# Performance work log

Hardware: AMD Instinct MI355X
Metric: run time of the kernel (lower is better)

The kernel has to match this reference:

```python
import jax, jax.numpy as jnp
import numpy as np

C = 256  # channels
B, H, W = 16, 64, 64


def _conv1x1(x, w, b):
    # x: [B,Cin,H,W], w: [Cout,Cin], b: [Cout] -> [B,Cout,H,W]
    return jnp.einsum('bchw,oc->bohw', x, w) + b[None, :, None, None]


def _axis_attn(x, wq, bq, wf, bf, axis):
    # axis: -1 for 'W', -2 for 'H'
    qkv = _conv1x1(x, wq, bq)                      # [B,1+2C,H,W]
    query = qkv[:, :1]                             # [B,1,H,W]
    key = qkv[:, 1:1 + C]                          # [B,C,H,W]
    value = qkv[:, 1 + C:]                         # [B,C,H,W]
    scores = jax.nn.softmax(query, axis=axis)      # softmax over spatial axis
    context = jnp.sum(key * scores, axis=axis, keepdims=True)  # [B,C,H,1] or [B,C,1,W]
    gate = jax.nn.sigmoid(value)
    out = x + gate * context                       # broadcast over reduced axis
    return _conv1x1(out, wf, bf)


def setup_inputs() -> dict:
    key = jax.random.key(0)
    ks = jax.random.split(key, 5)
    s_qkv = 1.0 / np.sqrt(C)
    s_fus = 1.0 / np.sqrt(C)
    return {
        'x': jax.random.normal(ks[0], (B, C, H, W), dtype=jnp.float32),
        'qkvW_w': jax.random.normal(ks[1], (1 + 2 * C, C), dtype=jnp.float32) * s_qkv,
        'qkvW_b': jnp.zeros((1 + 2 * C,), dtype=jnp.float32),
        'qkvH_w': jax.random.normal(ks[2], (1 + 2 * C, C), dtype=jnp.float32) * s_qkv,
        'qkvH_b': jnp.zeros((1 + 2 * C,), dtype=jnp.float32),
        'fusW_w': jax.random.normal(ks[3], (C, C), dtype=jnp.float32) * s_fus,
        'fusW_b': jnp.zeros((C,), dtype=jnp.float32),
        'fusH_w': jax.random.normal(ks[4], (C, C), dtype=jnp.float32) * s_fus,
        'fusH_b': jnp.zeros((C,), dtype=jnp.float32),
    }


def reference(x, qkvW_w, qkvW_b, qkvH_w, qkvH_b, fusW_w, fusW_b, fusH_w, fusH_b):
    x_w = _axis_attn(x, qkvW_w, qkvW_b, fusW_w, fusW_b, axis=-1)
    x_h = _axis_attn(x_w, qkvH_w, qkvH_b, fusH_w, fusH_b, axis=-2)
    return x_h
```

## Files before the change

### kernel.cpp

```cpp
#include <hip/hip_runtime.h>

typedef unsigned short u16;
typedef unsigned int u32;
typedef __attribute__((ext_vector_type(8))) short bf16x8;
typedef __attribute__((ext_vector_type(4))) float f32x4;

__device__ __forceinline__ u16 f2bf(float f) {
    u32 u = __builtin_bit_cast(u32, f);
    u += 0x7FFFu + ((u >> 16) & 1u);
    return (u16)(u >> 16);
}
__device__ __forceinline__ float bf2f(u16 s) {
    u32 u = ((u32)s) << 16;
    return __builtin_bit_cast(float, u);
}
__device__ __forceinline__ float sigm(float x) {
    return 1.0f / (1.0f + __expf(-x));
}
__device__ __forceinline__ void gload16(const u16* g, u16* l) {
    __builtin_amdgcn_global_load_lds(
        (const __attribute__((address_space(1))) void*)g,
        (__attribute__((address_space(3))) void*)l, 16, 0, 0);
}

__global__ __launch_bounds__(256) void transpose_in(const float* __restrict__ x,
                                                    u16* __restrict__ xp) {
    __shared__ float tile[64][65];
    int bid = blockIdx.x;
    int ct = bid & 3, h = (bid >> 2) & 63, b = bid >> 8;
    int t = threadIdx.x;
    int tr = t >> 4, tc = t & 15;
    const float* src = x + (((size_t)(b * 256 + ct * 64) * 64 + h) * 64);
#pragma unroll
    for (int i = 0; i < 4; ++i) {
        int c = tr + i * 16;
        float4 v = *(const float4*)(src + (size_t)c * 4096 + tc * 4);
        tile[c][tc * 4 + 0] = v.x;
        tile[c][tc * 4 + 1] = v.y;
        tile[c][tc * 4 + 2] = v.z;
        tile[c][tc * 4 + 3] = v.w;
    }
    __syncthreads();
    u16* dst = xp + ((size_t)((b * 64 + h) * 64)) * 256 + ct * 64;
#pragma unroll
    for (int i = 0; i < 4; ++i) {
        int w = tr + i * 16;
        ushort4 o;
        o.x = f2bf(tile[tc * 4 + 0][w]);
        o.y = f2bf(tile[tc * 4 + 1][w]);
        o.z = f2bf(tile[tc * 4 + 2][w]);
        o.w = f2bf(tile[tc * 4 + 3][w]);
        *(ushort4*)(dst + (size_t)w * 256 + tc * 4) = o;
    }
}

__global__ __launch_bounds__(256) void prep_w(const float* __restrict__ qw,
                                              const float* __restrict__ qb,
                                              const float* __restrict__ fw,
                                              const float* __restrict__ fb,
                                              float* __restrict__ wq0,
                                              u16* __restrict__ wkv,
                                              float* __restrict__ bkv,
                                              u16* __restrict__ wf,
                                              float* __restrict__ bff) {
    int i = blockIdx.x * 256 + threadIdx.x;
    if (i < 513 * 256) {
        int o = i >> 8, c = i & 255;
        float v = qw[i];
        if (o == 0) wq0[c] = v;
        else        wkv[(size_t)(o - 1) * 256 + c] = f2bf(v);
    }
    if (i < 65536) wf[i] = f2bf(fw[i]);
    if (i < 512)   bkv[i] = qb[i + 1];
    if (i < 256)   bff[i] = fb[i];
}

template <int AXIS>
__global__ __launch_bounds__(512, 2) void qkv_attn(
    const u16* __restrict__ A, const u16* __restrict__ Bw,
    const float* __restrict__ bkv, const float* __restrict__ wq0,
    u16* __restrict__ G) {
    __shared__ alignas(16) u16 Asm[128 * 256];
    __shared__ alignas(16) u16 Bsm[128 * 256];
    __shared__ float ql[128];
    __shared__ float sc[128];
    __shared__ float ctxs[2][256];
    int t = threadIdx.x, lane = t & 63, wv = t >> 6;
    int beta = blockIdx.x;
    auto prow = [&](int r) -> size_t {
        if (AXIS == 0) return (size_t)beta * 128 + r;
        else           return (size_t)(beta >> 5) * 4096 + (size_t)(r & 63) * 64 +
                              ((beta & 31) * 2) + (r >> 6);
    };
    {
        int r5 = t >> 5, c5 = t & 31;
#pragma unroll
        for (int i = 0; i < 8; ++i) {
            int row = i * 16 + r5;
            int slot = c5 ^ (row & 7);
            gload16(A + prow(row) * 256 + slot * 8, &Asm[(i * 16 + wv * 2) * 256]);
        }
    }
    __syncthreads();
    {
        int row = t >> 2, g = t & 3;
        const float* wp = wq0 + g * 64;
        float a = 0.f;
#pragma unroll
        for (int cc = 0; cc < 8; ++cc) {
            int slot = (g * 8 + cc) ^ (row & 7);
            bf16x8 v = *(const bf16x8*)&Asm[row * 256 + slot * 8];
#pragma unroll
            for (int j = 0; j < 8; ++j) a += bf2f((u16)v[j]) * wp[cc * 8 + j];
        }
        a += __shfl_xor(a, 1);
        a += __shfl_xor(a, 2);
        if (g == 0) ql[row] = a;
    }
    __syncthreads();
    if (t < 128) {
        float qv = ql[t];
        float m = qv;
#pragma unroll
        for (int off = 32; off > 0; off >>= 1) m = fmaxf(m, __shfl_xor(m, off));
        float e = __expf(qv - m);
        float s = e;
#pragma unroll
        for (int off = 32; off > 0; off >>= 1) s += __shfl_xor(s, off);
        sc[t] = e / s;
    }
    int wm = (wv & 1) * 64, wn = (wv >> 1) * 32;
    int arow = lane & 15, kgrp = lane >> 4, l7 = lane & 7;
    int line = wv & 1;
    for (int ot = 0; ot < 4; ++ot) {
        __syncthreads();
        {
            int r5 = t >> 5, c5 = t & 31;
#pragma unroll
            for (int i = 0; i < 8; ++i) {
                int row = i * 16 + r5;
                int slot = c5 ^ (row & 7);
                gload16(Bw + (size_t)(ot * 128 + row) * 256 + slot * 8,
                        &Bsm[(i * 16 + wv * 2) * 256]);
            }
        }
        __syncthreads();
        f32x4 zero = {0.f, 0.f, 0.f, 0.f};
        f32x4 acc[4][2];
#pragma unroll
        for (int mi = 0; mi < 4; ++mi) {
            acc[mi][0] = zero;
            acc[mi][1] = zero;
        }
#pragma unroll
        for (int ks = 0; ks < 8; ++ks) {
            int soff = ((ks * 4 + kgrp) ^ l7) * 8;
            bf16x8 af[4], bf[2];
#pragma unroll
            for (int mi = 0; mi < 4; ++mi)
                af[mi] = *(const bf16x8*)&Asm[(wm + mi * 16 + arow) * 256 + soff];
#pragma unroll
            for (int ni = 0; ni < 2; ++ni)
                bf[ni] = *(const bf16x8*)&Bsm[(wn + ni * 16 + arow) * 256 + soff];
#pragma unroll
            for (int mi = 0; mi < 4; ++mi)
#pragma unroll
                for (int ni = 0; ni < 2; ++ni)
                    acc[mi][ni] = __builtin_amdgcn_mfma_f32_16x16x32_bf16(
                        af[mi], bf[ni], acc[mi][ni], 0, 0, 0);
        }
        if (ot < 2) {
#pragma unroll
            for (int ni = 0; ni < 2; ++ni) {
                int col = ot * 128 + wn + ni * 16 + arow;
                float part = 0.f;
#pragma unroll
                for (int mi = 0; mi < 4; ++mi) {
                    int rbase = wm + mi * 16 + kgrp * 4;
#pragma unroll
                    for (int r = 0; r < 4; ++r)
                        part += acc[mi][ni][r] * sc[rbase + r];
                }
                part += __shfl_xor(part, 16);
                part += __shfl_xor(part, 32);
                if (lane < 16) ctxs[line][col] = part + bkv[col];
            }
        } else {
#pragma unroll
            for (int ni = 0; ni < 2; ++ni) {
                int c = (ot - 2) * 128 + wn + ni * 16 + arow;
                float bv = bkv[256 + c];
                float cx = ctxs[line][c];
#pragma unroll
                for (int mi = 0; mi < 4; ++mi) {
#pragma unroll
                    for (int r = 0; r < 4; ++r) {
                        int row = wm + mi * 16 + kgrp * 4 + r;
                        float v = acc[mi][ni][r] + bv;
                        int slot = (c >> 3) ^ (row & 7);
                        float xv = bf2f(Asm[row * 256 + slot * 8 + (c & 7)]);
                        G[prow(row) * 256 + c] = f2bf(xv + sigm(v) * cx);
                    }
                }
            }
        }
    }
}

template <int MODE>
__global__ __launch_bounds__(256, 2) void gemm_k(
    const u16* __restrict__ A, const u16* __restrict__ Bw,
    const float* __restrict__ bias,
    u16* __restrict__ bOut, float* __restrict__ fOut) {
    int h = blockIdx.x;
    int xcd = h & 7, slot = h >> 3;
    int otile = slot & 1, ptile = xcd * 64 + (slot >> 1);
    __shared__ alignas(16) u16 Asm[128 * 64];
    __shared__ alignas(16) u16 Bsm[128 * 64];
    int p0 = ptile * 128, o0 = otile * 128;
    int t = threadIdx.x, lane = t & 63, wv = t >> 6;
    int wm = (wv >> 1) * 64, wn = (wv & 1) * 64;
    int l7 = lane & 7;
    int srcoff = (lane >> 3) * 256 + (((lane & 7) ^ (lane >> 3)) * 8);
    int arow = lane & 15, kgrp = lane >> 4;
    f32x4 zero = {0.f, 0.f, 0.f, 0.f};
    f32x4 acc[4][4];
#pragma unroll
    for (int i = 0; i < 4; ++i)
#pragma unroll
        for (int jj = 0; jj < 4; ++jj) acc[i][jj] = zero;

    for (int k0 = 0; k0 < 256; k0 += 64) {
        __syncthreads();
#pragma unroll
        for (int it = 0; it < 4; ++it) {
            int r0 = it * 32 + wv * 8;
            gload16(A + (size_t)(p0 + r0) * 256 + k0 + srcoff, &Asm[r0 * 64]);
            gload16(Bw + (size_t)(o0 + r0) * 256 + k0 + srcoff, &Bsm[r0 * 64]);
        }
        __syncthreads();
#pragma unroll
        for (int kk = 0; kk < 64; kk += 32) {
            int soff = (((kk >> 3) + kgrp) ^ l7) << 3;
            bf16x8 af[4], bfv[4];
#pragma unroll
            for (int mi = 0; mi < 4; ++mi)
                af[mi] = *(const bf16x8*)&Asm[(wm + mi * 16 + arow) * 64 + soff];
#pragma unroll
            for (int ni = 0; ni < 4; ++ni)
                bfv[ni] = *(const bf16x8*)&Bsm[(wn + ni * 16 + arow) * 64 + soff];
#pragma unroll
            for (int mi = 0; mi < 4; ++mi)
#pragma unroll
                for (int ni = 0; ni < 4; ++ni)
                    acc[mi][ni] = __builtin_amdgcn_mfma_f32_16x16x32_bf16(
                        af[mi], bfv[ni], acc[mi][ni], 0, 0, 0);
        }
    }
#pragma unroll
    for (int mi = 0; mi < 4; ++mi) {
#pragma unroll
        for (int ni = 0; ni < 4; ++ni) {
            int col = o0 + wn + ni * 16 + arow;
            float bv = bias[col];
#pragma unroll
            for (int r = 0; r < 4; ++r) {
                int row = p0 + wm + mi * 16 + ((lane >> 4) << 2) + r;
                float v = acc[mi][ni][r] + bv;
                if (MODE == 1) {
                    bOut[(size_t)row * 256 + col] = f2bf(v);
                } else {
                    fOut[((size_t)((row >> 12) * 256 + col)) * 4096 + (row & 4095)] = v;
                }
            }
        }
    }
}

extern "C" void kernel_launch(void* const* d_in, const int* in_sizes, int n_in,
                              void* d_out, int out_size, void* d_ws, size_t ws_size,
                              hipStream_t stream) {
    const float* x   = (const float*)d_in[0];
    const float* qWw = (const float*)d_in[1];
    const float* qWb = (const float*)d_in[2];
    const float* qHw = (const float*)d_in[3];
    const float* qHb = (const float*)d_in[4];
    const float* fWw = (const float*)d_in[5];
    const float* fWb = (const float*)d_in[6];
    const float* fHw = (const float*)d_in[7];
    const float* fHb = (const float*)d_in[8];
    float* out = (float*)d_out;

    char* ws = (char*)d_ws;
    size_t off = 0;
    auto carve = [&](size_t bytes) -> void* {
        off = (off + 255) & ~(size_t)255;
        void* p = ws + off;
        off += bytes;
        return p;
    };
    const size_t P = 65536;
    u16*   xp  = (u16*)carve(P * 256 * 2);
    u16*   kb  = (u16*)carve(P * 256 * 2);
    u16*   vb  = (u16*)carve(P * 256 * 2);
    float* wq01 = (float*)carve(256 * 4);
    u16*   wkv1 = (u16*)carve(512 * 256 * 2);
    float* bkv1 = (float*)carve(512 * 4);
    u16*   wf1  = (u16*)carve(65536 * 2);
    float* bf1  = (float*)carve(256 * 4);
    float* wq02 = (float*)carve(256 * 4);
    u16*   wkv2 = (u16*)carve(512 * 256 * 2);
    float* bkv2 = (float*)carve(512 * 4);
    u16*   wf2  = (u16*)carve(65536 * 2);
    float* bf2  = (float*)carve(256 * 4);

    prep_w<<<513, 256, 0, stream>>>(qWw, qWb, fWw, fWb, wq01, wkv1, bkv1, wf1, bf1);
    prep_w<<<513, 256, 0, stream>>>(qHw, qHb, fHw, fHb, wq02, wkv2, bkv2, wf2, bf2);
    transpose_in<<<4096, 256, 0, stream>>>(x, xp);

    qkv_attn<0><<<512, 512, 0, stream>>>(xp, wkv1, bkv1, wq01, kb);
    gemm_k<1><<<1024, 256, 0, stream>>>(kb, wf1, bf1, vb, nullptr);
    qkv_attn<1><<<512, 512, 0, stream>>>(vb, wkv2, bkv2, wq02, kb);
    gemm_k<2><<<1024, 256, 0, stream>>>(kb, wf2, bf2, nullptr, out);
    (void)in_sizes; (void)n_in; (void)out_size; (void)ws_size;
}
```

Baseline: 160.6 us.

## Stream qkv weights from global memory and transpose MFMA operand roles in qkv_attn

Removes the 64KB shared-memory weight tile and the per-output-tile weight staging and barriers. Each wave now reads its weight fragments straight from global (L2-cached) memory as the MFMA A operand, with pixels as the B operand. This gives 4 consecutive channels per lane, so the gate epilogue can use vectorized ushort4 stores and f32x4 bias/context loads. Shared memory roughly halves, so launch bounds now ask for 4 blocks per CU. The trade-off is uncoalesced, latency-bound global loads inside the MFMA loop instead of LDS reads, and more registers spent on the transposed accumulator layout.

```diff
diff --git a/kernel.cpp b/kernel.cpp
--- a/kernel.cpp
+++ b/kernel.cpp
@@ -76,15 +76,14 @@
 }
 
 template <int AXIS>
-__global__ __launch_bounds__(512, 2) void qkv_attn(
+__global__ __launch_bounds__(512, 4) void qkv_attn(
     const u16* __restrict__ A, const u16* __restrict__ Bw,
     const float* __restrict__ bkv, const float* __restrict__ wq0,
     u16* __restrict__ G) {
     __shared__ alignas(16) u16 Asm[128 * 256];
-    __shared__ alignas(16) u16 Bsm[128 * 256];
     __shared__ float ql[128];
     __shared__ float sc[128];
-    __shared__ float ctxs[2][256];
+    __shared__ alignas(16) float ctxs[2][256];
     int t = threadIdx.x, lane = t & 63, wv = t >> 6;
     int beta = blockIdx.x;
     auto prow = [&](int r) -> size_t {
@@ -93,11 +92,10 @@
                               ((beta & 31) * 2) + (r >> 6);
     };
     {
-        int r5 = t >> 5, c5 = t & 31;
 #pragma unroll
         for (int i = 0; i < 8; ++i) {
-            int row = i * 16 + r5;
-            int slot = c5 ^ (row & 7);
+            int row = i * 16 + wv * 2 + (lane >> 5);
+            int slot = (lane & 31) ^ (row & 7);
             gload16(A + prow(row) * 256 + slot * 8, &Asm[(i * 16 + wv * 2) * 256]);
         }
     }
@@ -129,81 +127,84 @@
         for (int off = 32; off > 0; off >>= 1) s += __shfl_xor(s, off);
         sc[t] = e / s;
     }
-    int wm = (wv & 1) * 64, wn = (wv >> 1) * 32;
-    int arow = lane & 15, kgrp = lane >> 4, l7 = lane & 7;
-    int line = wv & 1;
+    __syncthreads();
+    int rowhalf = wv >> 2, chq = wv & 3;
+    int arow = lane & 15, kgrp = lane >> 4;
+    float sv[4];
+#pragma unroll
+    for (int ni = 0; ni < 4; ++ni) sv[ni] = sc[rowhalf * 64 + ni * 16 + arow];
     for (int ot = 0; ot < 4; ++ot) {
-        __syncthreads();
-        {
-            int r5 = t >> 5, c5 = t & 31;
-#pragma unroll
-            for (int i = 0; i < 8; ++i) {
-                int row = i * 16 + r5;
-                int slot = c5 ^ (row & 7);
-                gload16(Bw + (size_t)(ot * 128 + row) * 256 + slot * 8,
-                        &Bsm[(i * 16 + wv * 2) * 256]);
+        f32x4 zero = {0.f, 0.f, 0.f, 0.f};
+        f32x4 acc[2][4];
+#pragma unroll
+        for (int mi = 0; mi < 2; ++mi)
+#pragma unroll
+            for (int ni = 0; ni < 4; ++ni) acc[mi][ni] = zero;
+#pragma unroll
+        for (int ks = 0; ks < 8; ++ks) {
+            bf16x8 aw[2], bx[4];
+#pragma unroll
+            for (int mi = 0; mi < 2; ++mi)
+                aw[mi] = *(const bf16x8*)(Bw +
+                    (size_t)(ot * 128 + chq * 32 + mi * 16 + arow) * 256 +
+                    ks * 32 + kgrp * 8);
+#pragma unroll
+            for (int ni = 0; ni < 4; ++ni) {
+                int p = rowhalf * 64 + ni * 16 + arow;
+                int slot = (ks * 4 + kgrp) ^ (p & 7);
+                bx[ni] = *(const bf16x8*)&Asm[p * 256 + slot * 8];
             }
-        }
-        __syncthreads();
-        f32x4 zero = {0.f, 0.f, 0.f, 0.f};
-        f32x4 acc[4][2];
-#pragma unroll
-        for (int mi = 0; mi < 4; ++mi) {
-            acc[mi][0] = zero;
-            acc[mi][1] = zero;
-        }
-#pragma unroll
-        for (int ks = 0; ks < 8; ++ks) {
-            int soff = ((ks * 4 + kgrp) ^ l7) * 8;
-            bf16x8 af[4], bf[2];
-#pragma unroll
-            for (int mi = 0; mi < 4; ++mi)
-                af[mi] = *(const bf16x8*)&Asm[(wm + mi * 16 + arow) * 256 + soff];
-#pragma unroll
-            for (int ni = 0; ni < 2; ++ni)
-                bf[ni] = *(const bf16x8*)&Bsm[(wn + ni * 16 + arow) * 256 + soff];
-#pragma unroll
-            for (int mi = 0; mi < 4; ++mi)
-#pragma unroll
-                for (int ni = 0; ni < 2; ++ni)
+#pragma unroll
+            for (int mi = 0; mi < 2; ++mi)
+#pragma unroll
+                for (int ni = 0; ni < 4; ++ni)
                     acc[mi][ni] = __builtin_amdgcn_mfma_f32_16x16x32_bf16(
-                        af[mi], bf[ni], acc[mi][ni], 0, 0, 0);
+                        aw[mi], bx[ni], acc[mi][ni], 0, 0, 0);
         }
         if (ot < 2) {
 #pragma unroll
-            for (int ni = 0; ni < 2; ++ni) {
-                int col = ot * 128 + wn + ni * 16 + arow;
-                float part = 0.f;
-#pragma unroll
-                for (int mi = 0; mi < 4; ++mi) {
-                    int rbase = wm + mi * 16 + kgrp * 4;
-#pragma unroll
-                    for (int r = 0; r < 4; ++r)
-                        part += acc[mi][ni][r] * sc[rbase + r];
+            for (int mi = 0; mi < 2; ++mi) {
+                int c = ot * 128 + chq * 32 + mi * 16 + kgrp * 4;
+                f32x4 red;
+#pragma unroll
+                for (int r = 0; r < 4; ++r) {
+                    float s = 0.f;
+#pragma unroll
+                    for (int ni = 0; ni < 4; ++ni) s += acc[mi][ni][r] * sv[ni];
+                    s += __shfl_xor(s, 1);
+                    s += __shfl_xor(s, 2);
+                    s += __shfl_xor(s, 4);
+                    s += __shfl_xor(s, 8);
+                    red[r] = s;
                 }
-                part += __shfl_xor(part, 16);
-                part += __shfl_xor(part, 32);
-                if (lane < 16) ctxs[line][col] = part + bkv[col];
+                if (arow == 0) {
+                    f32x4 bv = *(const f32x4*)&bkv[c];
+                    red[0] += bv[0]; red[1] += bv[1];
+                    red[2] += bv[2]; red[3] += bv[3];
+                    *(f32x4*)&ctxs[rowhalf][c] = red;
+                }
             }
         } else {
 #pragma unroll
-            for (int ni = 0; ni < 2; ++ni) {
-                int c = (ot - 2) * 128 + wn + ni * 16 + arow;
-                float bv = bkv[256 + c];
-                float cx = ctxs[line][c];
-#pragma unroll
-                for (int mi = 0; mi < 4; ++mi) {
-#pragma unroll
-                    for (int r = 0; r < 4; ++r) {
-                        int row = wm + mi * 16 + kgrp * 4 + r;
-                        float v = acc[mi][ni][r] + bv;
-                        int slot = (c >> 3) ^ (row & 7);
-                        float xv = bf2f(Asm[row * 256 + slot * 8 + (c & 7)]);
-                        G[prow(row) * 256 + c] = f2bf(xv + sigm(v) * cx);
-                    }
+            for (int mi = 0; mi < 2; ++mi) {
+                int cv = (ot - 2) * 128 + chq * 32 + mi * 16 + kgrp * 4;
+                f32x4 bv = *(const f32x4*)&bkv[256 + cv];
+                f32x4 cxv = *(const f32x4*)&ctxs[rowhalf][cv];
+#pragma unroll
+                for (int ni = 0; ni < 4; ++ni) {
+                    int p = rowhalf * 64 + ni * 16 + arow;
+                    int slot = (cv >> 3) ^ (p & 7);
+                    ushort4 xv = *(const ushort4*)&Asm[p * 256 + slot * 8 + (cv & 7)];
+                    ushort4 o;
+                    o.x = f2bf(bf2f(xv.x) + sigm(acc[mi][ni][0] + bv[0]) * cxv[0]);
+                    o.y = f2bf(bf2f(xv.y) + sigm(acc[mi][ni][1] + bv[1]) * cxv[1]);
+                    o.z = f2bf(bf2f(xv.z) + sigm(acc[mi][ni][2] + bv[2]) * cxv[2]);
+                    o.w = f2bf(bf2f(xv.w) + sigm(acc[mi][ni][3] + bv[3]) * cxv[3]);
+                    *(ushort4*)(G + prow(p) * 256 + cv) = o;
                 }
             }
         }
+        if (ot == 1) __syncthreads();
     }
 }
 
```

New measurement: 159.1 us. No clear change (-0.9%).

## Compute attention context algebraically via softmax-weighted x then key weights

Applied to the files above, without the earlier changes.

Replaces the fused qkv_attn kernel with two kernels. line_ctx uses linearity: it first forms the softmax-weighted sum of x per line, then applies the key weights as a matrix-vector product, so the full key GEMM is never computed. val_gate then runs only the value GEMM with an MFMA-tiled loop and applies the sigmoid gate using the context read back from global memory. The change removes half the GEMM FLOPs in the attention stage, at the cost of an extra kernel launch, a second read of the activations and a small context buffer.

```diff
diff --git a/kernel.cpp b/kernel.cpp
--- a/kernel.cpp
+++ b/kernel.cpp
@@ -76,30 +76,25 @@
 }
 
 template <int AXIS>
-__global__ __launch_bounds__(512, 2) void qkv_attn(
-    const u16* __restrict__ A, const u16* __restrict__ Bw,
-    const float* __restrict__ bkv, const float* __restrict__ wq0,
-    u16* __restrict__ G) {
-    __shared__ alignas(16) u16 Asm[128 * 256];
-    __shared__ alignas(16) u16 Bsm[128 * 256];
-    __shared__ float ql[128];
-    __shared__ float sc[128];
-    __shared__ float ctxs[2][256];
+__global__ __launch_bounds__(256) void line_ctx(
+    const u16* __restrict__ A, const u16* __restrict__ Wk,
+    const float* __restrict__ wq0, const float* __restrict__ bkv,
+    float* __restrict__ ctx) {
+    __shared__ alignas(16) u16 Xl[64 * 256];
+    __shared__ float ql[64];
+    __shared__ float sc[64];
+    __shared__ alignas(16) float ys[256];
     int t = threadIdx.x, lane = t & 63, wv = t >> 6;
-    int beta = blockIdx.x;
+    int l = blockIdx.x;
     auto prow = [&](int r) -> size_t {
-        if (AXIS == 0) return (size_t)beta * 128 + r;
-        else           return (size_t)(beta >> 5) * 4096 + (size_t)(r & 63) * 64 +
-                              ((beta & 31) * 2) + (r >> 6);
+        if (AXIS == 0) return (size_t)l * 64 + r;
+        else           return (size_t)(l >> 6) * 4096 + (size_t)r * 64 + (l & 63);
     };
-    {
-        int r5 = t >> 5, c5 = t & 31;
-#pragma unroll
-        for (int i = 0; i < 8; ++i) {
-            int row = i * 16 + r5;
-            int slot = c5 ^ (row & 7);
-            gload16(A + prow(row) * 256 + slot * 8, &Asm[(i * 16 + wv * 2) * 256]);
-        }
+#pragma unroll
+    for (int i = 0; i < 8; ++i) {
+        int row = i * 8 + wv * 2 + (lane >> 5);
+        int slot = (lane & 31) ^ (row & 7);
+        gload16(A + prow(row) * 256 + slot * 8, &Xl[(i * 8 + wv * 2) * 256]);
     }
     __syncthreads();
     {
@@ -109,7 +104,7 @@
 #pragma unroll
         for (int cc = 0; cc < 8; ++cc) {
             int slot = (g * 8 + cc) ^ (row & 7);
-            bf16x8 v = *(const bf16x8*)&Asm[row * 256 + slot * 8];
+            bf16x8 v = *(const bf16x8*)&Xl[row * 256 + slot * 8];
 #pragma unroll
             for (int j = 0; j < 8; ++j) a += bf2f((u16)v[j]) * wp[cc * 8 + j];
         }
@@ -118,7 +113,7 @@
         if (g == 0) ql[row] = a;
     }
     __syncthreads();
-    if (t < 128) {
+    if (t < 64) {
         float qv = ql[t];
         float m = qv;
 #pragma unroll
@@ -129,79 +124,95 @@
         for (int off = 32; off > 0; off >>= 1) s += __shfl_xor(s, off);
         sc[t] = e / s;
     }
-    int wm = (wv & 1) * 64, wn = (wv >> 1) * 32;
-    int arow = lane & 15, kgrp = lane >> 4, l7 = lane & 7;
-    int line = wv & 1;
-    for (int ot = 0; ot < 4; ++ot) {
+    __syncthreads();
+    {
+        int chunk = t >> 3, e7 = t & 7;
+        float a = 0.f;
+#pragma unroll 8
+        for (int p = 0; p < 64; ++p) {
+            int slot = chunk ^ (p & 7);
+            a += bf2f(Xl[p * 256 + slot * 8 + e7]) * sc[p];
+        }
+        ys[t] = a;
+    }
+    __syncthreads();
+    {
+        const u16* wk = Wk + (size_t)t * 256;
+        float a = 0.f;
+#pragma unroll
+        for (int kc = 0; kc < 32; ++kc) {
+            bf16x8 w = *(const bf16x8*)(wk + kc * 8);
+#pragma unroll
+            for (int j = 0; j < 8; ++j) a += bf2f((u16)w[j]) * ys[kc * 8 + j];
+        }
+        ctx[(size_t)l * 256 + t] = a + bkv[t];
+    }
+}
+
+template <int AXIS>
+__global__ __launch_bounds__(256, 2) void val_gate(
+    const u16* __restrict__ A, const u16* __restrict__ Wv,
+    const float* __restrict__ bv, const float* __restrict__ ctx,
+    u16* __restrict__ G) {
+    int h = blockIdx.x;
+    int xcd = h & 7, slot = h >> 3;
+    int otile = slot & 1, ptile = xcd * 64 + (slot >> 1);
+    __shared__ alignas(16) u16 Asm[128 * 64];
+    __shared__ alignas(16) u16 Bsm[128 * 64];
+    int p0 = ptile * 128, o0 = otile * 128;
+    int t = threadIdx.x, lane = t & 63, wv = t >> 6;
+    int wm = (wv >> 1) * 64, wn = (wv & 1) * 64;
+    int l7 = lane & 7;
+    int srcoff = (lane >> 3) * 256 + (((lane & 7) ^ (lane >> 3)) * 8);
+    int arow = lane & 15, kgrp = lane >> 4;
+    f32x4 zero = {0.f, 0.f, 0.f, 0.f};
+    f32x4 acc[4][4];
+#pragma unroll
+    for (int i = 0; i < 4; ++i)
+#pragma unroll
+        for (int jj = 0; jj < 4; ++jj) acc[i][jj] = zero;
+
+    for (int k0 = 0; k0 < 256; k0 += 64) {
         __syncthreads();
-        {
-            int r5 = t >> 5, c5 = t & 31;
-#pragma unroll
-            for (int i = 0; i < 8; ++i) {
-                int row = i * 16 + r5;
-                int slot = c5 ^ (row & 7);
-                gload16(Bw + (size_t)(ot * 128 + row) * 256 + slot * 8,
-                        &Bsm[(i * 16 + wv * 2) * 256]);
-            }
+#pragma unroll
+        for (int it = 0; it < 4; ++it) {
+            int r0 = it * 32 + wv * 8;
+            gload16(A + (size_t)(p0 + r0) * 256 + k0 + srcoff, &Asm[r0 * 64]);
+            gload16(Wv + (size_t)(o0 + r0) * 256 + k0 + srcoff, &Bsm[r0 * 64]);
         }
         __syncthreads();
-        f32x4 zero = {0.f, 0.f, 0.f, 0.f};
-        f32x4 acc[4][2];
-#pragma unroll
-        for (int mi = 0; mi < 4; ++mi) {
-            acc[mi][0] = zero;
-            acc[mi][1] = zero;
-        }
-#pragma unroll
-        for (int ks = 0; ks < 8; ++ks) {
-            int soff = ((ks * 4 + kgrp) ^ l7) * 8;
-            bf16x8 af[4], bf[2];
+#pragma unroll
+        for (int kk = 0; kk < 64; kk += 32) {
+            int soff = (((kk >> 3) + kgrp) ^ l7) << 3;
+            bf16x8 af[4], bfv[4];
 #pragma unroll
             for (int mi = 0; mi < 4; ++mi)
-                af[mi] = *(const bf16x8*)&Asm[(wm + mi * 16 + arow) * 256 + soff];
-#pragma unroll
-            for (int ni = 0; ni < 2; ++ni)
-                bf[ni] = *(const bf16x8*)&Bsm[(wn + ni * 16 + arow) * 256 + soff];
+                af[mi] = *(const bf16x8*)&Asm[(wm + mi * 16 + arow) * 64 + soff];
+#pragma unroll
+            for (int ni = 0; ni < 4; ++ni)
+                bfv[ni] = *(const bf16x8*)&Bsm[(wn + ni * 16 + arow) * 64 + soff];
 #pragma unroll
             for (int mi = 0; mi < 4; ++mi)
 #pragma unroll
-                for (int ni = 0; ni < 2; ++ni)
+                for (int ni = 0; ni < 4; ++ni)
                     acc[mi][ni] = __builtin_amdgcn_mfma_f32_16x16x32_bf16(
-                        af[mi], bf[ni], acc[mi][ni], 0, 0, 0);
-        }
-        if (ot < 2) {
-#pragma unroll
-            for (int ni = 0; ni < 2; ++ni) {
-                int col = ot * 128 + wn + ni * 16 + arow;
-                float part = 0.f;
-#pragma unroll
-                for (int mi = 0; mi < 4; ++mi) {
-                    int rbase = wm + mi * 16 + kgrp * 4;
-#pragma unroll
-                    for (int r = 0; r < 4; ++r)
-                        part += acc[mi][ni][r] * sc[rbase + r];
-                }
-                part += __shfl_xor(part, 16);
-                part += __shfl_xor(part, 32);
-                if (lane < 16) ctxs[line][col] = part + bkv[col];
-            }
-        } else {
-#pragma unroll
-            for (int ni = 0; ni < 2; ++ni) {
-                int c = (ot - 2) * 128 + wn + ni * 16 + arow;
-                float bv = bkv[256 + c];
-                float cx = ctxs[line][c];
-#pragma unroll
-                for (int mi = 0; mi < 4; ++mi) {
-#pragma unroll
-                    for (int r = 0; r < 4; ++r) {
-                        int row = wm + mi * 16 + kgrp * 4 + r;
-                        float v = acc[mi][ni][r] + bv;
-                        int slot = (c >> 3) ^ (row & 7);
-                        float xv = bf2f(Asm[row * 256 + slot * 8 + (c & 7)]);
-                        G[prow(row) * 256 + c] = f2bf(xv + sigm(v) * cx);
-                    }
-                }
+                        af[mi], bfv[ni], acc[mi][ni], 0, 0, 0);
+        }
+    }
+#pragma unroll
+    for (int mi = 0; mi < 4; ++mi) {
+#pragma unroll
+        for (int ni = 0; ni < 4; ++ni) {
+            int col = o0 + wn + ni * 16 + arow;
+            float bias = bv[col];
+#pragma unroll
+            for (int r = 0; r < 4; ++r) {
+                int row = p0 + wm + mi * 16 + (kgrp << 2) + r;
+                int line = (AXIS == 0) ? (row >> 6) : ((row >> 12) * 64 + (row & 63));
+                float cx = ctx[(size_t)line * 256 + col];
+                float xv = bf2f(A[(size_t)row * 256 + col]);
+                float v = acc[mi][ni][r] + bias;
+                G[(size_t)row * 256 + col] = f2bf(xv + sigm(v) * cx);
             }
         }
     }
@@ -303,6 +314,7 @@
     u16*   xp  = (u16*)carve(P * 256 * 2);
     u16*   kb  = (u16*)carve(P * 256 * 2);
     u16*   vb  = (u16*)carve(P * 256 * 2);
+    float* ctxb = (float*)carve(1024 * 256 * 4);
     float* wq01 = (float*)carve(256 * 4);
     u16*   wkv1 = (u16*)carve(512 * 256 * 2);
     float* bkv1 = (float*)carve(512 * 4);
@@ -318,9 +330,13 @@
     prep_w<<<513, 256, 0, stream>>>(qHw, qHb, fHw, fHb, wq02, wkv2, bkv2, wf2, bf2);
     transpose_in<<<4096, 256, 0, stream>>>(x, xp);
 
-    qkv_attn<0><<<512, 512, 0, stream>>>(xp, wkv1, bkv1, wq01, kb);
+    line_ctx<0><<<1024, 256, 0, stream>>>(xp, wkv1, wq01, bkv1, ctxb);
+    val_gate<0><<<1024, 256, 0, stream>>>(xp, wkv1 + 256 * 256, bkv1 + 256,
+                                          ctxb, kb);
     gemm_k<1><<<1024, 256, 0, stream>>>(kb, wf1, bf1, vb, nullptr);
-    qkv_attn<1><<<512, 512, 0, stream>>>(vb, wkv2, bkv2, wq02, kb);
+    line_ctx<1><<<1024, 256, 0, stream>>>(vb, wkv2, wq02, bkv2, ctxb);
+    val_gate<1><<<1024, 256, 0, stream>>>(vb, wkv2 + 256 * 256, bkv2 + 256,
+                                          ctxb, kb);
     gemm_k<2><<<1024, 256, 0, stream>>>(kb, wf2, bf2, nullptr, out);
     (void)in_sizes; (void)n_in; (void)out_size; (void)ws_size;
 }
```

Result: slower. 167.3 us (+4.2%).
